# Kernel tuning notes

Hardware: AMD Instinct MI355X
Metric: run time of the kernel (lower is better)

The kernel has to match this reference:

```python
import jax, jax.numpy as jnp
import numpy as np

ALPHA = 0.2    # LeakyReLU negative slope (init arg alpha)
HEADS = 8
EPS = 1e-5     # LayerNorm eps


def setup_inputs() -> dict:
    key = jax.random.key(0)
    ks = jax.random.split(key, 16)
    B, S, D = 4, 1024, 256
    dh = D // HEADS  # 32
    x = jax.random.normal(ks[0], (B, S, D), jnp.float32)
    adj = (jax.random.uniform(ks[1], (B, S, S)) < 0.05).astype(jnp.float32)
    adj = jnp.maximum(adj, jnp.eye(S, dtype=jnp.float32)[None])

    def w(k, shape, fan):
        return jax.random.normal(k, shape, jnp.float32) * (fan ** -0.5)

    # GAT layer 0: in->hidden (concat heads)
    W0 = w(ks[2], (D, D), D); a_src0 = w(ks[3], (HEADS, dh), dh); a_dst0 = w(ks[4], (HEADS, dh), dh)
    # GAT layer 1: hidden->hidden (concat heads)
    W1 = w(ks[5], (D, D), D); a_src1 = w(ks[6], (HEADS, dh), dh); a_dst1 = w(ks[7], (HEADS, dh), dh)
    # GAT layer 2: hidden->out (mean over heads, head_dim = out_dim)
    W2 = w(ks[8], (D, HEADS * D), D); a_src2 = w(ks[9], (HEADS, D), D); a_dst2 = w(ks[10], (HEADS, D), D)
    # LayerNorm
    ln_g = jnp.ones((D,), jnp.float32); ln_b = jnp.zeros((D,), jnp.float32)
    # FFN: D -> 2D -> D
    ff_w1 = w(ks[11], (D, 2 * D), D); ff_b1 = jnp.zeros((2 * D,), jnp.float32)
    ff_w2 = w(ks[12], (2 * D, D), 2 * D); ff_b2 = jnp.zeros((D,), jnp.float32)
    return dict(adj=adj, x=x, W0=W0, a_src0=a_src0, a_dst0=a_dst0,
                W1=W1, a_src1=a_src1, a_dst1=a_dst1,
                W2=W2, a_src2=a_src2, a_dst2=a_dst2,
                ln_g=ln_g, ln_b=ln_b,
                ff_w1=ff_w1, ff_b1=ff_b1, ff_w2=ff_w2, ff_b2=ff_b2)


def _gat_layer(h, adj, W, a_src, a_dst, concat):
    B, S, _ = h.shape
    hp = jnp.einsum('bsi,io->bso', h, W).reshape(B, S, HEADS, -1)  # [B,S,H,dh]
    src = jnp.einsum('bshd,hd->bsh', hp, a_src)  # per-node source score
    dst = jnp.einsum('bshd,hd->bsh', hp, a_dst)  # per-node dest score
    # e[b,i,j,h] = LeakyReLU(src_i + dst_j), masked by adjacency
    e = jax.nn.leaky_relu(src[:, :, None, :] + dst[:, None, :, :], ALPHA)
    e = jnp.where(adj[..., None] > 0, e, jnp.float32(-1e9))
    attn = jax.nn.softmax(e, axis=2)  # softmax over neighbors j
    out = jnp.einsum('bijh,bjhd->bihd', attn, hp)
    return out.reshape(B, S, -1) if concat else out.mean(axis=2)


def reference(adj, x, W0, a_src0, a_dst0, W1, a_src1, a_dst1, W2, a_src2, a_dst2,
              ln_g, ln_b, ff_w1, ff_b1, ff_w2, ff_b2):
    # MultiAttentionGAT: 3 layers with residuals, ELU between layers
    h = jax.nn.elu(_gat_layer(x, adj, W0, a_src0, a_dst0, True) + x)
    h = jax.nn.elu(_gat_layer(h, adj, W1, a_src1, a_dst1, True) + h)
    h = _gat_layer(h, adj, W2, a_src2, a_dst2, False) + h
    # LayerNorm
    mu = h.mean(-1, keepdims=True)
    var = h.var(-1, keepdims=True)
    h = (h - mu) * jax.lax.rsqrt(var + EPS) * ln_g + ln_b
    # GELU FFN + residual
    ff = jnp.dot(jax.nn.gelu(jnp.dot(h, ff_w1) + ff_b1), ff_w2) + ff_b2
    return h + ff
```

## Files before the change

kernel.cpp:

```cpp
#include <hip/hip_runtime.h>
#include <hip/hip_bf16.h>

#define B_ 4
#define S_ 1024
#define D_ 256
#define H_ 8
#define LRELU_ALPHA 0.2f
#define MAXDEG 128

typedef __attribute__((ext_vector_type(8))) short short8;
typedef __attribute__((ext_vector_type(4))) float floatx4;

__device__ __forceinline__ float bf2f(unsigned short u) {
    union { unsigned int i; float f; } c; c.i = ((unsigned int)u) << 16; return c.f;
}
__device__ __forceinline__ unsigned short f2bf(float f) {
    union { float f; unsigned int u; } c; c.f = f;
    unsigned int r = (c.u + 0x7FFF + ((c.u >> 16) & 1)) >> 16;
    return (unsigned short)r;
}

__device__ void castT_body(const float* __restrict__ W, unsigned short* __restrict__ out,
                           int K, int N, int k0, int n0, float (*t)[33], int tid) {
    int tx = tid & 31, ty = tid >> 5;
#pragma unroll
    for (int i = 0; i < 4; ++i)
        t[ty + 8 * i][tx] = W[(size_t)(k0 + ty + 8 * i) * N + n0 + tx];
    __syncthreads();
#pragma unroll
    for (int i = 0; i < 4; ++i)
        out[(size_t)(n0 + ty + 8 * i) * K + k0 + tx] = f2bf(t[tx][ty + 8 * i]);
}

__global__ __launch_bounds__(256) void k_prep(
        const float* __restrict__ x, unsigned short* __restrict__ xb,
        const float* __restrict__ W0, unsigned short* __restrict__ W0t,
        const float* __restrict__ W1, unsigned short* __restrict__ W1t,
        const float* __restrict__ W2, unsigned short* __restrict__ W2t,
        const float* __restrict__ F1, unsigned short* __restrict__ F1t,
        const float* __restrict__ F2, unsigned short* __restrict__ F2t,
        const float* __restrict__ as2, const float* __restrict__ ad2,
        float* __restrict__ WS2, float* __restrict__ WD2,
        const float* __restrict__ adj, int* __restrict__ nbr, int* __restrict__ cnt) {
    __shared__ float t[32][33];
    __shared__ int c;
    int b = blockIdx.x, tid = threadIdx.x;
    if (b < 1024) {
        int i = b * 256 + tid;
        float4 v = ((const float4*)x)[i];
        ushort4 u; u.x = f2bf(v.x); u.y = f2bf(v.y); u.z = f2bf(v.z); u.w = f2bf(v.w);
        ((ushort4*)xb)[i] = u;
    } else if (b < 1088) {
        int i = b - 1024; castT_body(W0, W0t, 256, 256, (i & 7) * 32, (i >> 3) * 32, t, tid);
    } else if (b < 1152) {
        int i = b - 1088; castT_body(W1, W1t, 256, 256, (i & 7) * 32, (i >> 3) * 32, t, tid);
    } else if (b < 1664) {
        int i = b - 1152;
        int k0 = (i & 7) * 32, d0 = ((i >> 3) & 7) * 32, h = i >> 6;
        int tx = tid & 31, ty = tid >> 5;
#pragma unroll
        for (int q = 0; q < 4; ++q)
            t[ty + 8 * q][tx] = W2[(size_t)(k0 + ty + 8 * q) * 2048 + h * 256 + d0 + tx];
        __syncthreads();
#pragma unroll
        for (int q = 0; q < 4; ++q)
            W2t[(size_t)(d0 + ty + 8 * q) * 2048 + h * 256 + k0 + tx] = f2bf(t[tx][ty + 8 * q]);
    } else if (b < 1792) {
        int i = b - 1664; castT_body(F1, F1t, 256, 512, (i & 7) * 32, (i >> 3) * 32, t, tid);
    } else if (b < 1920) {
        int i = b - 1792; castT_body(F2, F2t, 512, 256, (i & 15) * 32, (i >> 4) * 32, t, tid);
    } else if (b < 1928) {
        int h = b - 1920, k = tid;
        const float* wrow = W2 + (size_t)k * 2048 + h * 256;
        float s = 0.f, d = 0.f;
        for (int dd = 0; dd < 256; ++dd) {
            float w = wrow[dd];
            s += w * as2[h * 256 + dd];
            d += w * ad2[h * 256 + dd];
        }
        WS2[h * 256 + k] = s;
        WD2[h * 256 + k] = d;
    } else {
        int row = b - 1928;
        if (tid == 0) c = 0;
        __syncthreads();
        float4 a4 = ((const float4*)(adj + (size_t)row * S_))[tid];
#pragma unroll
        for (int q = 0; q < 4; ++q) {
            float a = q == 0 ? a4.x : q == 1 ? a4.y : q == 2 ? a4.z : a4.w;
            if (a > 0.f) {
                int s = atomicAdd(&c, 1);
                if (s < MAXDEG) nbr[row * MAXDEG + s] = tid * 4 + q;
            }
        }
        __syncthreads();
        if (tid == 0) cnt[row] = c < MAXDEG ? c : MAXDEG;
    }
}

__global__ __launch_bounds__(256) void k_gemm_wide(const unsigned short* __restrict__ A,
        const unsigned short* __restrict__ Bt, float* __restrict__ P,
        int M, int N, int K, int Kc) {
    __shared__ unsigned short As[64][40];
    __shared__ unsigned short Bs[256][40];
    int tid = threadIdx.x;
    int bm = blockIdx.y * 64, bn = blockIdx.x * 256;
    int kbeg = blockIdx.z * Kc, kend = kbeg + Kc;
    int lane = tid & 63, wv = tid >> 6;
    int lrow = lane & 15, lq = lane >> 4;
    floatx4 acc[4][4] = {};
    int sm = tid >> 2, skq = (tid & 3) * 8;
    const unsigned short* Ap = A + (size_t)(bm + sm) * K + skq;
    const unsigned short* Bp0 = Bt + (size_t)(bn + sm) * K + skq;
    const unsigned short* Bp1 = Bp0 + (size_t)64 * K;
    const unsigned short* Bp2 = Bp0 + (size_t)128 * K;
    const unsigned short* Bp3 = Bp0 + (size_t)192 * K;
    short8 av  = *(const short8*)(Ap + kbeg);
    short8 bv0 = *(const short8*)(Bp0 + kbeg);
    short8 bv1 = *(const short8*)(Bp1 + kbeg);
    short8 bv2 = *(const short8*)(Bp2 + kbeg);
    short8 bv3 = *(const short8*)(Bp3 + kbeg);
    for (int k0 = kbeg; k0 < kend; k0 += 32) {
        *(short8*)&As[sm][skq]        = av;
        *(short8*)&Bs[sm][skq]        = bv0;
        *(short8*)&Bs[sm + 64][skq]   = bv1;
        *(short8*)&Bs[sm + 128][skq]  = bv2;
        *(short8*)&Bs[sm + 192][skq]  = bv3;
        __syncthreads();
        if (k0 + 32 < kend) {
            av  = *(const short8*)(Ap + k0 + 32);
            bv0 = *(const short8*)(Bp0 + k0 + 32);
            bv1 = *(const short8*)(Bp1 + k0 + 32);
            bv2 = *(const short8*)(Bp2 + k0 + 32);
            bv3 = *(const short8*)(Bp3 + k0 + 32);
        }
        short8 aF[4], bF[4];
#pragma unroll
        for (int mi = 0; mi < 4; ++mi)
            aF[mi] = *(const short8*)&As[mi * 16 + lrow][lq * 8];
#pragma unroll
        for (int ni = 0; ni < 4; ++ni)
            bF[ni] = *(const short8*)&Bs[wv * 64 + ni * 16 + lrow][lq * 8];
#pragma unroll
        for (int mi = 0; mi < 4; ++mi)
#pragma unroll
            for (int ni = 0; ni < 4; ++ni)
                acc[mi][ni] = __builtin_amdgcn_mfma_f32_16x16x32_bf16(aF[mi], bF[ni], acc[mi][ni], 0, 0, 0);
        __syncthreads();
    }
    float* out = P + (size_t)blockIdx.z * M * N;
#pragma unroll
    for (int mi = 0; mi < 4; ++mi)
#pragma unroll
        for (int ni = 0; ni < 4; ++ni)
#pragma unroll
            for (int r = 0; r < 4; ++r) {
                int grow = bm + mi * 16 + lq * 4 + r;
                int gcol = bn + wv * 64 + ni * 16 + lrow;
                out[(size_t)grow * N + gcol] = acc[mi][ni][r];
            }
}

template<int EPI>
__global__ __launch_bounds__(256) void k_gemm64(
        const unsigned short* __restrict__ A, const unsigned short* __restrict__ Bt,
        int N, int K,
        float* __restrict__ Pout, unsigned short* __restrict__ Ob,
        const float* __restrict__ p1, const float* __restrict__ p2,
        float* __restrict__ SRC, float* __restrict__ DST) {
    __shared__ unsigned short As[64][40];
    __shared__ unsigned short Bs[64][40];
    int tid = threadIdx.x;
    int bm = blockIdx.y * 64, bn = blockIdx.x * 64;
    int lane = tid & 63, wv = tid >> 6;
    int lrow = lane & 15, lq = lane >> 4;
    floatx4 acc[4] = {};
    int sm = tid >> 2, skq = (tid & 3) * 8;
    const unsigned short* Ap = A + (size_t)(bm + sm) * K + skq;
    const unsigned short* Bp = Bt + (size_t)(bn + sm) * K + skq;
    short8 av = *(const short8*)Ap;
    short8 bv = *(const short8*)Bp;
    for (int k0 = 0; k0 < K; k0 += 32) {
        *(short8*)&As[sm][skq] = av;
        *(short8*)&Bs[sm][skq] = bv;
        __syncthreads();
        if (k0 + 32 < K) {
            av = *(const short8*)(Ap + k0 + 32);
            bv = *(const short8*)(Bp + k0 + 32);
        }
        short8 aF = *(const short8*)&As[wv * 16 + lrow][lq * 8];
        short8 bF[4];
#pragma unroll
        for (int ni = 0; ni < 4; ++ni)
            bF[ni] = *(const short8*)&Bs[ni * 16 + lrow][lq * 8];
#pragma unroll
        for (int ni = 0; ni < 4; ++ni)
            acc[ni] = __builtin_amdgcn_mfma_f32_16x16x32_bf16(aF, bF[ni], acc[ni], 0, 0, 0);
        __syncthreads();
    }
    int row0 = bm + wv * 16 + lq * 4;
    if (EPI == 0) {
#pragma unroll
        for (int ni = 0; ni < 4; ++ni)
#pragma unroll
            for (int r = 0; r < 4; ++r)
                Ob[(size_t)(row0 + r) * N + bn + ni * 16 + lrow] = f2bf(acc[ni][r]);
        float asv[4], adv[4];
#pragma unroll
        for (int ni = 0; ni < 4; ++ni) {
            asv[ni] = p1[bn + ni * 16 + lrow];
            adv[ni] = p2[bn + ni * 16 + lrow];
        }
#pragma unroll
        for (int r = 0; r < 4; ++r) {
            float sA = acc[0][r] * asv[0] + acc[1][r] * asv[1];
            float sB = acc[2][r] * asv[2] + acc[3][r] * asv[3];
            float dA = acc[0][r] * adv[0] + acc[1][r] * adv[1];
            float dB = acc[2][r] * adv[2] + acc[3][r] * adv[3];
#pragma unroll
            for (int o = 8; o; o >>= 1) {
                sA += __shfl_xor(sA, o); sB += __shfl_xor(sB, o);
                dA += __shfl_xor(dA, o); dB += __shfl_xor(dB, o);
            }
            if (lrow == 0) {
                int h0 = bn >> 5;
                SRC[(row0 + r) * 8 + h0]     = sA;
                SRC[(row0 + r) * 8 + h0 + 1] = sB;
                DST[(row0 + r) * 8 + h0]     = dA;
                DST[(row0 + r) * 8 + h0 + 1] = dB;
            }
        }
    } else if (EPI == 2) {
#pragma unroll
        for (int ni = 0; ni < 4; ++ni) {
            int gcol = bn + ni * 16 + lrow;
            float bb = p1[gcol];
#pragma unroll
            for (int r = 0; r < 4; ++r) {
                float xx = acc[ni][r] + bb;
                float tt = tanhf(0.7978845608028654f * (xx + 0.044715f * xx * xx * xx));
                Ob[(size_t)(row0 + r) * N + gcol] = f2bf(0.5f * xx * (1.f + tt));
            }
        }
    } else if (EPI == 3) {
#pragma unroll
        for (int ni = 0; ni < 4; ++ni) {
            int gcol = bn + ni * 16 + lrow;
            float bb = p1[gcol];
#pragma unroll
            for (int r = 0; r < 4; ++r) {
                float res = p2[(size_t)(row0 + r) * 256 + gcol];
                Pout[(size_t)(row0 + r) * 256 + gcol] = acc[ni][r] + bb + res;
            }
        }
    }
}

__global__ __launch_bounds__(256) void k_attn_small_f(const unsigned short* __restrict__ hp,
        const float* __restrict__ src, const float* __restrict__ dst,
        const int* __restrict__ nbr, const int* __restrict__ cnts,
        const float* __restrict__ X, float* __restrict__ Hout,
        unsigned short* __restrict__ Hb,
        const float* __restrict__ WS2, const float* __restrict__ WD2,
        float* __restrict__ SRC2, float* __restrict__ DST2) {
    int tid = threadIdx.x;
    int half = tid >> 7;
    int sub = tid & 127;
    int row = blockIdx.x * 2 + half;
    int rb = row & ~(S_ - 1);
    __shared__ int nb[2][MAXDEG];
    __shared__ float ss[2][8];
    __shared__ float ew[2][MAXDEG * 9];
    __shared__ float pr[2][2][16];
    int cnt = cnts[row];
    for (int t = sub; t < cnt; t += 128) nb[half][t] = nbr[row * MAXDEG + t];
    if (sub < 8) ss[half][sub] = src[row * H_ + sub];
    __syncthreads();
    for (int idx = sub; idx < cnt * 8; idx += 128) {
        int n = idx >> 3, h = idx & 7;
        int j = nb[half][n];
        float e = ss[half][h] + dst[(rb + j) * H_ + h];
        ew[half][n * 9 + h] = e > 0.f ? e : LRELU_ALPHA * e;
    }
    __syncthreads();
    {
        int wv2 = sub >> 6, lane = sub & 63;
        int h = wv2 * 4 + (lane >> 4), s16 = lane & 15;
        float m = -1e30f;
        for (int n = s16; n < cnt; n += 16) m = fmaxf(m, ew[half][n * 9 + h]);
        for (int o = 8; o; o >>= 1) m = fmaxf(m, __shfl_xor(m, o));
        float s = 0.f;
        for (int n = s16; n < cnt; n += 16) {
            float v = __expf(ew[half][n * 9 + h] - m); ew[half][n * 9 + h] = v; s += v;
        }
        for (int o = 8; o; o >>= 1) s += __shfl_xor(s, o);
        float inv = s > 0.f ? 1.f / s : 0.f;
        for (int n = s16; n < cnt; n += 16) ew[half][n * 9 + h] *= inv;
    }
    __syncthreads();
    int d0 = sub * 2;
    int h = sub >> 4;
    const unsigned short* hpb = hp + (size_t)rb * 256 + d0;
    const float* ewr = ew[half];
    float aA0 = 0.f, aA1 = 0.f, aB0 = 0.f, aB1 = 0.f;
    float aC0 = 0.f, aC1 = 0.f, aD0 = 0.f, aD1 = 0.f;
    int n = 0;
    for (; n + 3 < cnt; n += 4) {
        int j0 = nb[half][n], j1 = nb[half][n + 1];
        int j2 = nb[half][n + 2], j3 = nb[half][n + 3];
        unsigned int p0 = *(const unsigned int*)(hpb + (size_t)j0 * 256);
        unsigned int p1 = *(const unsigned int*)(hpb + (size_t)j1 * 256);
        unsigned int p2 = *(const unsigned int*)(hpb + (size_t)j2 * 256);
        unsigned int p3 = *(const unsigned int*)(hpb + (size_t)j3 * 256);
        float w0 = ewr[n * 9 + h], w1 = ewr[(n + 1) * 9 + h];
        float w2 = ewr[(n + 2) * 9 + h], w3 = ewr[(n + 3) * 9 + h];
        aA0 += w0 * bf2f((unsigned short)p0); aA1 += w0 * bf2f((unsigned short)(p0 >> 16));
        aB0 += w1 * bf2f((unsigned short)p1); aB1 += w1 * bf2f((unsigned short)(p1 >> 16));
        aC0 += w2 * bf2f((unsigned short)p2); aC1 += w2 * bf2f((unsigned short)(p2 >> 16));
        aD0 += w3 * bf2f((unsigned short)p3); aD1 += w3 * bf2f((unsigned short)(p3 >> 16));
    }
    for (; n < cnt; ++n) {
        int j = nb[half][n];
        unsigned int p = *(const unsigned int*)(hpb + (size_t)j * 256);
        float w = ewr[n * 9 + h];
        aA0 += w * bf2f((unsigned short)p); aA1 += w * bf2f((unsigned short)(p >> 16));
    }
    float2 xv = *(const float2*)(X + (size_t)row * 256 + d0);
    float ov0 = (aA0 + aB0) + (aC0 + aD0) + xv.x;
    float ov1 = (aA1 + aB1) + (aC1 + aD1) + xv.y;
    ov0 = ov0 > 0.f ? ov0 : (__expf(ov0) - 1.f);
    ov1 = ov1 > 0.f ? ov1 : (__expf(ov1) - 1.f);
    *(float2*)(Hout + (size_t)row * 256 + d0) = make_float2(ov0, ov1);
    ushort2 ub; ub.x = f2bf(ov0); ub.y = f2bf(ov1);
    *(ushort2*)(Hb + (size_t)row * 256 + d0) = ub;
    if (WS2 != nullptr) {
        int wv2 = sub >> 6, lane = sub & 63;
#pragma unroll
        for (int hh = 0; hh < 8; ++hh) {
            float sP = ov0 * WS2[hh * 256 + d0] + ov1 * WS2[hh * 256 + d0 + 1];
            float dP = ov0 * WD2[hh * 256 + d0] + ov1 * WD2[hh * 256 + d0 + 1];
            for (int o = 32; o; o >>= 1) { sP += __shfl_xor(sP, o); dP += __shfl_xor(dP, o); }
            if (lane == 0) { pr[half][wv2][hh * 2] = sP; pr[half][wv2][hh * 2 + 1] = dP; }
        }
        __syncthreads();
        if (sub < 16) {
            float tv = pr[half][0][sub] + pr[half][1][sub];
            if ((sub & 1) == 0) SRC2[row * 8 + (sub >> 1)] = tv;
            else                DST2[row * 8 + (sub >> 1)] = tv;
        }
    }
}

__global__ __launch_bounds__(256) void k_attn_Y(const unsigned short* __restrict__ Hb,
        const float* __restrict__ src2, const float* __restrict__ dst2,
        const int* __restrict__ nbr, const int* __restrict__ cnts,
        unsigned short* __restrict__ Ycat) {
    int row = blockIdx.x;
    int tid = threadIdx.x;
    int rb = row & ~(S_ - 1);
    __shared__ int nb[MAXDEG];
    __shared__ float ss[8];
    __shared__ float ew[MAXDEG * 8];
    int cnt = cnts[row];
    for (int t = tid; t < cnt; t += 256) nb[t] = nbr[row * MAXDEG + t];
    if (tid < 8) ss[tid] = src2[row * H_ + tid];
    __syncthreads();
    for (int idx = tid; idx < cnt * 8; idx += 256) {
        int n = idx >> 3, h = idx & 7;
        int j = nb[n];
        float e = ss[h] + dst2[(rb + j) * H_ + h];
        ew[n * 8 + h] = e > 0.f ? e : LRELU_ALPHA * e;
    }
    __syncthreads();
    {
        int lane = tid & 63, wv = tid >> 6;
        int h = wv * 2 + (lane >> 5), sub = lane & 31;
        float m = -1e30f;
        for (int n = sub; n < cnt; n += 32) m = fmaxf(m, ew[n * 8 + h]);
        for (int o = 16; o; o >>= 1) m = fmaxf(m, __shfl_xor(m, o));
        float s = 0.f;
        for (int n = sub; n < cnt; n += 32) {
            float v = __expf(ew[n * 8 + h] - m); ew[n * 8 + h] = v; s += v;
        }
        for (int o = 16; o; o >>= 1) s += __shfl_xor(s, o);
        float inv = s > 0.f ? 0.125f / s : 0.f;
        for (int n = sub; n < cnt; n += 32) ew[n * 8 + h] *= inv;
    }
    __syncthreads();
    int dp = tid & 127, hg = tid >> 7;
    const unsigned short* hbase = Hb + (size_t)rb * 256 + 2 * dp;
    const float* ewh = ew + hg * 4;
    float a0x = 0.f, a0y = 0.f, a0z = 0.f, a0w = 0.f;
    float a1x = 0.f, a1y = 0.f, a1z = 0.f, a1w = 0.f;
    int n = 0;
    for (; n + 3 < cnt; n += 4) {
        int j0 = nb[n], j1 = nb[n + 1], j2 = nb[n + 2], j3 = nb[n + 3];
        unsigned int p0 = *(const unsigned int*)(hbase + (size_t)j0 * 256);
        unsigned int p1 = *(const unsigned int*)(hbase + (size_t)j1 * 256);
        unsigned int p2 = *(const unsigned int*)(hbase + (size_t)j2 * 256);
        unsigned int p3 = *(const unsigned int*)(hbase + (size_t)j3 * 256);
        float4 w0 = *(const float4*)(ewh + n * 8);
        float4 w1 = *(const float4*)(ewh + (n + 1) * 8);
        float4 w2 = *(const float4*)(ewh + (n + 2) * 8);
        float4 w3 = *(const float4*)(ewh + (n + 3) * 8);
        float v0a = bf2f((unsigned short)p0), v0b = bf2f((unsigned short)(p0 >> 16));
        float v1a = bf2f((unsigned short)p1), v1b = bf2f((unsigned short)(p1 >> 16));
        float v2a = bf2f((unsigned short)p2), v2b = bf2f((unsigned short)(p2 >> 16));
        float v3a = bf2f((unsigned short)p3), v3b = bf2f((unsigned short)(p3 >> 16));
        a0x += w0.x * v0a + w1.x * v1a + w2.x * v2a + w3.x * v3a;
        a0y += w0.y * v0a + w1.y * v1a + w2.y * v2a + w3.y * v3a;
        a0z += w0.z * v0a + w1.z * v1a + w2.z * v2a + w3.z * v3a;
        a0w += w0.w * v0a + w1.w * v1a + w2.w * v2a + w3.w * v3a;
        a1x += w0.x * v0b + w1.x * v1b + w2.x * v2b + w3.x * v3b;
        a1y += w0.y * v0b + w1.y * v1b + w2.y * v2b + w3.y * v3b;
        a1z += w0.z * v0b + w1.z * v1b + w2.z * v2b + w3.z * v3b;
        a1w += w0.w * v0b + w1.w * v1b + w2.w * v2b + w3.w * v3b;
    }
    for (; n < cnt; ++n) {
        int j = nb[n];
        unsigned int p = *(const unsigned int*)(hbase + (size_t)j * 256);
        float4 w = *(const float4*)(ewh + n * 8);
        float va = bf2f((unsigned short)p), vb = bf2f((unsigned short)(p >> 16));
        a0x += w.x * va; a0y += w.y * va; a0z += w.z * va; a0w += w.w * va;
        a1x += w.x * vb; a1y += w.y * vb; a1z += w.z * vb; a1w += w.w * vb;
    }
    unsigned short* yb = Ycat + (size_t)row * 2048 + (hg * 4) * 256 + 2 * dp;
    ushort2 u;
    u.x = f2bf(a0x); u.y = f2bf(a1x); *(ushort2*)(yb)         = u;
    u.x = f2bf(a0y); u.y = f2bf(a1y); *(ushort2*)(yb + 256)   = u;
    u.x = f2bf(a0z); u.y = f2bf(a1z); *(ushort2*)(yb + 512)   = u;
    u.x = f2bf(a0w); u.y = f2bf(a1w); *(ushort2*)(yb + 768)   = u;
}

__global__ __launch_bounds__(256) void k_ln_red(const float* __restrict__ P, int nsplit,
        const float* __restrict__ Hres, const float* __restrict__ g,
        const float* __restrict__ bta, float* __restrict__ HLN,
        unsigned short* __restrict__ HLNb) {
    int row = blockIdx.x * 4 + (threadIdx.x >> 6);
    int lane = threadIdx.x & 63;
    float4 v = ((const float4*)(Hres + (size_t)row * 256))[lane];
    for (int sp = 0; sp < nsplit; ++sp) {
        float4 p = ((const float4*)(P + (size_t)sp * 1048576 + (size_t)row * 256))[lane];
        v.x += p.x; v.y += p.y; v.z += p.z; v.w += p.w;
    }
    float s = v.x + v.y + v.z + v.w;
    float q = v.x * v.x + v.y * v.y + v.z * v.z + v.w * v.w;
    for (int o = 32; o; o >>= 1) { s += __shfl_xor(s, o); q += __shfl_xor(q, o); }
    float mu = s * (1.f / 256.f);
    float var = q * (1.f / 256.f) - mu * mu;
    if (var < 0.f) var = 0.f;
    float rs = rsqrtf(var + 1e-5f);
    float4 gg = ((const float4*)g)[lane];
    float4 bb = ((const float4*)bta)[lane];
    float4 o;
    o.x = (v.x - mu) * rs * gg.x + bb.x;
    o.y = (v.y - mu) * rs * gg.y + bb.y;
    o.z = (v.z - mu) * rs * gg.z + bb.z;
    o.w = (v.w - mu) * rs * gg.w + bb.w;
    ((float4*)(HLN + (size_t)row * 256))[lane] = o;
    ushort4 ob; ob.x = f2bf(o.x); ob.y = f2bf(o.y); ob.z = f2bf(o.z); ob.w = f2bf(o.w);
    ((ushort4*)(HLNb + (size_t)row * 256))[lane] = ob;
}

extern "C" void kernel_launch(void* const* d_in, const int* in_sizes, int n_in,
                              void* d_out, int out_size, void* d_ws, size_t ws_size,
                              hipStream_t stream) {
    const float* adj   = (const float*)d_in[0];
    const float* x     = (const float*)d_in[1];
    const float* W0    = (const float*)d_in[2];
    const float* as0   = (const float*)d_in[3];
    const float* ad0   = (const float*)d_in[4];
    const float* W1    = (const float*)d_in[5];
    const float* as1   = (const float*)d_in[6];
    const float* ad1   = (const float*)d_in[7];
    const float* W2    = (const float*)d_in[8];
    const float* as2   = (const float*)d_in[9];
    const float* ad2   = (const float*)d_in[10];
    const float* ln_g  = (const float*)d_in[11];
    const float* ln_b  = (const float*)d_in[12];
    const float* ff_w1 = (const float*)d_in[13];
    const float* ff_b1 = (const float*)d_in[14];
    const float* ff_w2 = (const float*)d_in[15];
    const float* ff_b2 = (const float*)d_in[16];

    float* ws = (float*)d_ws;
    float* H    = ws;
    float* HLN  = ws + 1048576;
    unsigned short* Ycat = (unsigned short*)(ws + 2097152);
    unsigned short* HPb  = (unsigned short*)(ws + 6291456);
    unsigned short* xb   = (unsigned short*)(ws + 6815744);
    unsigned short* Hb   = (unsigned short*)(ws + 7340032);
    unsigned short* HLNb = (unsigned short*)(ws + 7864320);
    unsigned short* MIDb = (unsigned short*)(ws + 8388608);
    unsigned short* W0t  = (unsigned short*)(ws + 9437184);
    unsigned short* W1t  = (unsigned short*)(ws + 9469952);
    unsigned short* W2t  = (unsigned short*)(ws + 9502720);
    unsigned short* F1t  = (unsigned short*)(ws + 9764864);
    unsigned short* F2t  = (unsigned short*)(ws + 9830400);
    float* WS2  = ws + 9895936;
    float* WD2  = ws + 9897984;
    float* SRC  = ws + 9900032;
    float* DST  = ws + 9932800;
    float* SRC2 = ws + 9965568;
    float* DST2 = ws + 9998336;
    int*   NBR  = (int*)(ws + 10031104);
    int*   CNT  = (int*)(ws + 10555392);
    float* PP   = ws + 12582912;

    k_prep<<<6024, 256, 0, stream>>>(x, xb, W0, W0t, W1, W1t, W2, W2t,
                                     ff_w1, F1t, ff_w2, F2t, as2, ad2, WS2, WD2,
                                     adj, NBR, CNT);

    k_gemm64<0><<<dim3(4, 64), 256, 0, stream>>>(xb, W0t, 256, 256,
                                                 nullptr, HPb, as0, ad0, SRC, DST);
    k_attn_small_f<<<2048, 256, 0, stream>>>(HPb, SRC, DST, NBR, CNT, x, H, Hb,
                                             nullptr, nullptr, nullptr, nullptr);

    k_gemm64<0><<<dim3(4, 64), 256, 0, stream>>>(Hb, W1t, 256, 256,
                                                 nullptr, HPb, as1, ad1, SRC, DST);
    k_attn_small_f<<<2048, 256, 0, stream>>>(HPb, SRC, DST, NBR, CNT, H, H, Hb,
                                             WS2, WD2, SRC2, DST2);

    k_attn_Y<<<4096, 256, 0, stream>>>(Hb, SRC2, DST2, NBR, CNT, Ycat);
    k_gemm_wide<<<dim3(1, 64, 4), 256, 0, stream>>>(Ycat, W2t, PP, 4096, 256, 2048, 512);
    k_ln_red<<<1024, 256, 0, stream>>>(PP, 4, H, ln_g, ln_b, HLN, HLNb);

    k_gemm64<2><<<dim3(8, 64), 256, 0, stream>>>(HLNb, F1t, 512, 256,
                                                 nullptr, MIDb, ff_b1, nullptr, nullptr, nullptr);
    k_gemm64<3><<<dim3(4, 64), 256, 0, stream>>>(MIDb, F2t, 256, 512,
                                                 (float*)d_out, nullptr, ff_b2, HLN, nullptr, nullptr);
}
```

Baseline: 218.3 us.

## Parallelize W2 score-projection prep, double-buffer gemm64 LDS, widen split-K

The W2 attention-score projection in the prep kernel was computed by 8 blocks with serial 256-long loops per thread. It now runs across 512 blocks, with one wavefront per output doing float4 loads and a shuffle reduction, which removes a long serial tail from the prep launch. The 64x64 GEMM now double-buffers its LDS tiles, cutting one barrier per K step. The wide GEMM's split-K goes from 4 to 8 slices, raising parallelism at the cost of more partial sums for the LayerNorm reduction to read.

```diff
diff --git a/kernel.cpp b/kernel.cpp
--- a/kernel.cpp
+++ b/kernel.cpp
@@ -69,19 +69,20 @@
         int i = b - 1664; castT_body(F1, F1t, 256, 512, (i & 7) * 32, (i >> 3) * 32, t, tid);
     } else if (b < 1920) {
         int i = b - 1792; castT_body(F2, F2t, 512, 256, (i & 15) * 32, (i >> 4) * 32, t, tid);
-    } else if (b < 1928) {
-        int h = b - 1920, k = tid;
-        const float* wrow = W2 + (size_t)k * 2048 + h * 256;
-        float s = 0.f, d = 0.f;
-        for (int dd = 0; dd < 256; ++dd) {
-            float w = wrow[dd];
-            s += w * as2[h * 256 + dd];
-            d += w * ad2[h * 256 + dd];
-        }
-        WS2[h * 256 + k] = s;
-        WD2[h * 256 + k] = d;
+    } else if (b < 2432) {
+        int id = (b - 1920) * 4 + (tid >> 6);
+        int h = id >> 8, k = id & 255;
+        int lane = tid & 63;
+        float4 w4 = *(const float4*)(W2 + (size_t)k * 2048 + h * 256 + lane * 4);
+        float4 a4 = *(const float4*)(as2 + h * 256 + lane * 4);
+        float4 d4 = *(const float4*)(ad2 + h * 256 + lane * 4);
+        float s = w4.x * a4.x + w4.y * a4.y + w4.z * a4.z + w4.w * a4.w;
+        float d = w4.x * d4.x + w4.y * d4.y + w4.z * d4.z + w4.w * d4.w;
+#pragma unroll
+        for (int o = 32; o; o >>= 1) { s += __shfl_xor(s, o); d += __shfl_xor(d, o); }
+        if (lane == 0) { WS2[h * 256 + k] = s; WD2[h * 256 + k] = d; }
     } else {
-        int row = b - 1928;
+        int row = b - 2432;
         if (tid == 0) c = 0;
         __syncthreads();
         float4 a4 = ((const float4*)(adj + (size_t)row * S_))[tid];
@@ -168,8 +169,8 @@
         float* __restrict__ Pout, unsigned short* __restrict__ Ob,
         const float* __restrict__ p1, const float* __restrict__ p2,
         float* __restrict__ SRC, float* __restrict__ DST) {
-    __shared__ unsigned short As[64][40];
-    __shared__ unsigned short Bs[64][40];
+    __shared__ unsigned short As[2][64][40];
+    __shared__ unsigned short Bs[2][64][40];
     int tid = threadIdx.x;
     int bm = blockIdx.y * 64, bn = blockIdx.x * 64;
     int lane = tid & 63, wv = tid >> 6;
@@ -180,23 +181,30 @@
     const unsigned short* Bp = Bt + (size_t)(bn + sm) * K + skq;
     short8 av = *(const short8*)Ap;
     short8 bv = *(const short8*)Bp;
+    *(short8*)&As[0][sm][skq] = av;
+    *(short8*)&Bs[0][sm][skq] = bv;
+    __syncthreads();
+    int cur = 0;
     for (int k0 = 0; k0 < K; k0 += 32) {
-        *(short8*)&As[sm][skq] = av;
-        *(short8*)&Bs[sm][skq] = bv;
-        __syncthreads();
-        if (k0 + 32 < K) {
+        bool more = k0 + 32 < K;
+        if (more) {
             av = *(const short8*)(Ap + k0 + 32);
             bv = *(const short8*)(Bp + k0 + 32);
         }
-        short8 aF = *(const short8*)&As[wv * 16 + lrow][lq * 8];
+        short8 aF = *(const short8*)&As[cur][wv * 16 + lrow][lq * 8];
         short8 bF[4];
 #pragma unroll
         for (int ni = 0; ni < 4; ++ni)
-            bF[ni] = *(const short8*)&Bs[ni * 16 + lrow][lq * 8];
+            bF[ni] = *(const short8*)&Bs[cur][ni * 16 + lrow][lq * 8];
 #pragma unroll
         for (int ni = 0; ni < 4; ++ni)
             acc[ni] = __builtin_amdgcn_mfma_f32_16x16x32_bf16(aF, bF[ni], acc[ni], 0, 0, 0);
-        __syncthreads();
+        if (more) {
+            *(short8*)&As[cur ^ 1][sm][skq] = av;
+            *(short8*)&Bs[cur ^ 1][sm][skq] = bv;
+            __syncthreads();
+            cur ^= 1;
+        }
     }
     int row0 = bm + wv * 16 + lq * 4;
     if (EPI == 0) {
@@ -507,7 +515,7 @@
     int*   CNT  = (int*)(ws + 10555392);
     float* PP   = ws + 12582912;
 
-    k_prep<<<6024, 256, 0, stream>>>(x, xb, W0, W0t, W1, W1t, W2, W2t,
+    k_prep<<<6528, 256, 0, stream>>>(x, xb, W0, W0t, W1, W1t, W2, W2t,
                                      ff_w1, F1t, ff_w2, F2t, as2, ad2, WS2, WD2,
                                      adj, NBR, CNT);
 
@@ -522,8 +530,8 @@
                                              WS2, WD2, SRC2, DST2);
 
     k_attn_Y<<<4096, 256, 0, stream>>>(Hb, SRC2, DST2, NBR, CNT, Ycat);
-    k_gemm_wide<<<dim3(1, 64, 4), 256, 0, stream>>>(Ycat, W2t, PP, 4096, 256, 2048, 512);
-    k_ln_red<<<1024, 256, 0, stream>>>(PP, 4, H, ln_g, ln_b, HLN, HLNb);
+    k_gemm_wide<<<dim3(1, 64, 8), 256, 0, stream>>>(Ycat, W2t, PP, 4096, 256, 2048, 256);
+    k_ln_red<<<1024, 256, 0, stream>>>(PP, 8, H, ln_g, ln_b, HLN, HLNb);
 
     k_gemm64<2><<<dim3(8, 64), 256, 0, stream>>>(HLNb, F1t, 512, 256,
                                                  nullptr, MIDb, ff_b1, nullptr, nullptr, nullptr);
```

After: 215.5 us. Within noise of the previous version (-1.3%).
